# Optimization experiments

Hardware: AMD Instinct MI355X
Metric: run time of the kernel (lower is better)

The kernel has to match this reference:

```python
import jax, jax.numpy as jnp
import numpy as np
from jax.ops import segment_sum

N_V = 50000   # vertices
N_E = 10000   # hyperedges
N_P = 800000  # incidence pairs
D_IN = 256
D_OUT = 256
NEG_SLOPE = 0.01


def setup_inputs() -> dict:
    key = jax.random.key(0)
    k1, k2, k3, k4, k5 = jax.random.split(key, 5)
    X = jax.random.normal(k1, (N_V, D_IN), dtype=jnp.float32)
    W = jax.random.normal(k2, (D_IN, D_OUT), dtype=jnp.float32) * (1.0 / np.sqrt(D_IN))
    b = jax.random.normal(k3, (D_OUT,), dtype=jnp.float32) * 0.01
    v_idx = jax.random.randint(k4, (N_P,), 0, N_V, dtype=jnp.int32)
    e_idx = jax.random.randint(k5, (N_P,), 0, N_E, dtype=jnp.int32)
    return {"X": X, "W": W, "b": b, "v_idx": v_idx, "e_idx": e_idx,
            "num_hyperedges": N_E}


def _mean_scatter(msg, idx, num_segments):
    # segment mean with count clamped to >=1 (empty segments -> 0)
    s = segment_sum(msg, idx, num_segments=num_segments)
    cnt = segment_sum(jnp.ones((msg.shape[0],), msg.dtype), idx,
                      num_segments=num_segments)
    return s / jnp.maximum(cnt, 1.0)[:, None]


def reference(X, W, b, v_idx, e_idx, num_hyperedges):
    # theta: linear projection  [N_V, D_OUT]
    H = X @ W + b
    # v2e mean: hyperedge features from member vertices
    e_feat = _mean_scatter(H[v_idx], e_idx, num_hyperedges)   # [N_E, D_OUT]
    # e2v mean: vertex features from incident hyperedges
    v_feat = _mean_scatter(e_feat[e_idx], v_idx, X.shape[0])  # [N_V, D_OUT]
    # leaky relu, default negative slope 0.01
    return jnp.where(v_feat >= 0, v_feat, NEG_SLOPE * v_feat)
```

## Files before the change

### kernel.cpp

```cpp
#include <hip/hip_runtime.h>

#define D 256
#define NEG_SLOPE 0.01f
#define E_PAD 192
#define V_PAD 64
#define EB 32
#define VB 64
#define NBE 313
#define NBV 782
#define CAP_E 3328
#define CAP_V 1536
#define CHUNK 1024
#define CR (CHUNK/256)
#define NS 8
#define DS 32
#define NSE 2
#define DSE 128

__device__ __forceinline__ unsigned short f2bf(float f) {
    union { float f; unsigned u; } x; x.f = f;
    unsigned r = x.u + 0x7fffu + ((x.u >> 16) & 1u);
    return (unsigned short)(r >> 16);
}
__device__ __forceinline__ void acc8(float* acc, uint4 g) {
    union { unsigned u; float f; } t;
    t.u = g.x << 16;         acc[0] += t.f;
    t.u = g.x & 0xffff0000u; acc[1] += t.f;
    t.u = g.y << 16;         acc[2] += t.f;
    t.u = g.y & 0xffff0000u; acc[3] += t.f;
    t.u = g.z << 16;         acc[4] += t.f;
    t.u = g.z & 0xffff0000u; acc[5] += t.f;
    t.u = g.w << 16;         acc[6] += t.f;
    t.u = g.w & 0xffff0000u; acc[7] += t.f;
}

__global__ __launch_bounds__(256) void prep_kernel(
        const float* __restrict__ X, unsigned short* __restrict__ Xhs,
        const int* __restrict__ v_idx, const int* __restrict__ e_idx,
        int* __restrict__ bc_e, int* __restrict__ bc_v,
        unsigned* __restrict__ pe, unsigned* __restrict__ pv,
        int n_v, int n_p, int gp) {
    __shared__ int he[NBE], hv[NBV], beb[NBE], bvb[NBV];
    const int tid = threadIdx.x;
    if ((int)blockIdx.x < gp) {
        const int base = (int)blockIdx.x * CHUNK;
        int le[CR], lv[CR];
        for (int i = tid; i < NBE; i += 256) he[i] = 0;
        for (int i = tid; i < NBV; i += 256) hv[i] = 0;
        __syncthreads();
        #pragma unroll
        for (int r = 0; r < CR; ++r) {
            int p = base + r * 256 + tid;
            le[r] = -1; lv[r] = -1;
            if (p < n_p) {
                le[r] = e_idx[p]; lv[r] = v_idx[p];
                atomicAdd(&he[le[r] >> 5], 1);
                atomicAdd(&hv[lv[r] >> 6], 1);
            }
        }
        __syncthreads();
        for (int b = tid; b < NBE; b += 256) {
            int c = he[b];
            beb[b] = c ? atomicAdd(&bc_e[b], c) : 0;
            he[b] = 0;
        }
        for (int b = tid; b < NBV; b += 256) {
            int c = hv[b];
            bvb[b] = c ? atomicAdd(&bc_v[b], c) : 0;
            hv[b] = 0;
        }
        __syncthreads();
        #pragma unroll
        for (int r = 0; r < CR; ++r) {
            if (le[r] >= 0) {
                int e = le[r], v = lv[r];
                int b1 = e >> 5;
                int s1 = beb[b1] + atomicAdd(&he[b1], 1);
                if (s1 < CAP_E) pe[(size_t)b1 * CAP_E + s1] = (unsigned)v | ((unsigned)e << 16);
                int b2 = v >> 6;
                int s2 = bvb[b2] + atomicAdd(&hv[b2], 1);
                if (s2 < CAP_V) pv[(size_t)b2 * CAP_V + s2] = (unsigned)e | ((unsigned)v << 16);
            }
        }
    } else {
        int i = ((int)blockIdx.x - gp) * 256 + tid;
        if (i >= n_v * 64) return;
        int v = i >> 6;
        int d4 = (i & 63) * 4;
        float4 val = *(const float4*)(X + (size_t)v * D + d4);
        ushort4 h;
        h.x = f2bf(val.x); h.y = f2bf(val.y); h.z = f2bf(val.z); h.w = f2bf(val.w);
        int s = d4 >> 5, wd = d4 & 31;
        *(ushort4*)(Xhs + (size_t)s * n_v * DS + (size_t)v * DS + wd) = h;
    }
}

__global__ __launch_bounds__(256) void build_kernel(
        const unsigned* __restrict__ pe, const unsigned* __restrict__ pv,
        const int* __restrict__ bc_e, const int* __restrict__ bc_v,
        unsigned short* __restrict__ e_adj, int* __restrict__ e_fill,
        unsigned short* __restrict__ v_adj, int* __restrict__ v_fill,
        int n_e, int n_v) {
    __shared__ unsigned short adj[EB * E_PAD];
    __shared__ int cnt[VB];
    const int tid = threadIdx.x;
    if ((int)blockIdx.x < NBE) {
        const int b = blockIdx.x;
        const int e0 = b * EB;
        int m = n_e - e0; if (m > EB) m = EB;
        for (int i = tid; i < EB; i += 256) cnt[i] = 0;
        __syncthreads();
        int total = bc_e[b]; if (total > CAP_E) total = CAP_E;
        for (int i = tid; i < total; i += 256) {
            unsigned p = pe[(size_t)b * CAP_E + i];
            int v = (int)(p & 0xFFFFu);
            int el = (int)(p >> 16) - e0;
            int s = atomicAdd(&cnt[el], 1);
            if (s < E_PAD) adj[el * E_PAD + s] = (unsigned short)v;
        }
        __syncthreads();
        unsigned* gout = (unsigned*)(e_adj + (size_t)e0 * E_PAD);
        const unsigned* lin = (const unsigned*)adj;
        int words = m * E_PAD / 2;
        for (int j = tid; j < words; j += 256) gout[j] = lin[j];
        for (int el = tid; el < m; el += 256) {
            int c = cnt[el]; if (c > E_PAD) c = E_PAD;
            e_fill[e0 + el] = c;
        }
    } else {
        const int b = (int)blockIdx.x - NBE;
        const int v0 = b * VB;
        int m = n_v - v0; if (m > VB) m = VB;
        for (int i = tid; i < VB; i += 256) cnt[i] = 0;
        __syncthreads();
        int total = bc_v[b]; if (total > CAP_V) total = CAP_V;
        for (int i = tid; i < total; i += 256) {
            unsigned p = pv[(size_t)b * CAP_V + i];
            int e = (int)(p & 0xFFFFu);
            int vl = (int)(p >> 16) - v0;
            int s = atomicAdd(&cnt[vl], 1);
            if (s < V_PAD) adj[vl * V_PAD + s] = (unsigned short)e;
        }
        __syncthreads();
        unsigned* gout = (unsigned*)(v_adj + (size_t)v0 * V_PAD);
        const unsigned* lin = (const unsigned*)adj;
        int words = m * V_PAD / 2;
        for (int j = tid; j < words; j += 256) gout[j] = lin[j];
        for (int vl = tid; vl < m; vl += 256) {
            int c = cnt[vl]; if (c > V_PAD) c = V_PAD;
            v_fill[v0 + vl] = c;
        }
    }
}

__global__ __launch_bounds__(256) void v2e_kernel(
        const unsigned short* __restrict__ Xhs, const int* __restrict__ e_fill,
        const unsigned short* __restrict__ e_adj, float* __restrict__ Xagg,
        int n_e, int n_v) {
    const int s    = blockIdx.x;
    const int eg   = threadIdx.x >> 4;
    const int l16  = threadIdx.x & 15;
    const int ph   = l16 >> 2;
    const int sub  = l16 & 3;
    const int e    = blockIdx.y * 16 + eg;
    if (e >= n_e) return;
    const unsigned short* tab = Xhs + (size_t)s * n_v * DS + (sub << 3);
    const unsigned short* adj = e_adj + (size_t)e * E_PAD;
    int cnt = e_fill[e]; if (cnt > E_PAD) cnt = E_PAD;
    float acc[8] = {};
    int i = ph * 4;
    for (; i + 4 <= cnt; i += 16) {
        ushort4 A = *(const ushort4*)(adj + i);
        uint4 g0 = *(const uint4*)(tab + (size_t)A.x * DS);
        uint4 g1 = *(const uint4*)(tab + (size_t)A.y * DS);
        uint4 g2 = *(const uint4*)(tab + (size_t)A.z * DS);
        uint4 g3 = *(const uint4*)(tab + (size_t)A.w * DS);
        acc8(acc, g0); acc8(acc, g1); acc8(acc, g2); acc8(acc, g3);
    }
    for (int j = i; j < cnt; ++j) {
        uint4 g = *(const uint4*)(tab + (size_t)adj[j] * DS);
        acc8(acc, g);
    }
    #pragma unroll
    for (int k = 0; k < 8; ++k) {
        acc[k] += __shfl_xor(acc[k], 4);
        acc[k] += __shfl_xor(acc[k], 8);
    }
    if (ph == 0) {
        int c = cnt < 1 ? 1 : cnt;
        float inv = 1.0f / (float)c;
        float4 o0, o1;
        o0.x = acc[0] * inv; o0.y = acc[1] * inv; o0.z = acc[2] * inv; o0.w = acc[3] * inv;
        o1.x = acc[4] * inv; o1.y = acc[5] * inv; o1.z = acc[6] * inv; o1.w = acc[7] * inv;
        float* orow = Xagg + (size_t)e * D + s * DS + (sub << 3);
        *(float4*)(orow)     = o0;
        *(float4*)(orow + 4) = o1;
    }
}

#define BM 64
#define BN 64
#define BK 64
#define SAK 68
#define SBN 68

__global__ __launch_bounds__(256) void gemm_kernel(
        const float* __restrict__ A, const float* __restrict__ B,
        const float* __restrict__ bias, const int* __restrict__ e_cnt,
        unsigned short* __restrict__ Ehs, int M) {
    __shared__ float As[BM * SAK];
    __shared__ float Bs[BK * SBN];
    const int tid = threadIdx.x;
    const int tx = tid & 15, ty = tid >> 4;
    const int m0 = blockIdx.y * BM;
    const int n0 = blockIdx.x * BN;

    float acc[4][4] = {};

    for (int k0 = 0; k0 < D; k0 += BK) {
        #pragma unroll
        for (int r = 0; r < 4; ++r) {
            int l  = (tid + r * 256) * 4;
            int am = l >> 6;
            int ak = l & 63;
            int grow = m0 + am;
            float4 v = make_float4(0.f, 0.f, 0.f, 0.f);
            if (grow < M) v = *(const float4*)(A + (size_t)grow * D + k0 + ak);
            *(float4*)(&As[am * SAK + ak]) = v;
        }
        #pragma unroll
        for (int r = 0; r < 4; ++r) {
            int l  = (tid + r * 256) * 4;
            int bk = l >> 6;
            int bn = l & 63;
            float4 v = *(const float4*)(B + (size_t)(k0 + bk) * D + n0 + bn);
            *(float4*)(&Bs[bk * SBN + bn]) = v;
        }
        __syncthreads();

        #pragma unroll 8
        for (int kk = 0; kk < BK; ++kk) {
            float a0 = As[(ty * 4 + 0) * SAK + kk];
            float a1 = As[(ty * 4 + 1) * SAK + kk];
            float a2 = As[(ty * 4 + 2) * SAK + kk];
            float a3 = As[(ty * 4 + 3) * SAK + kk];
            float4 bv = *(const float4*)(Bs + kk * SBN + tx * 4);
            acc[0][0] += a0 * bv.x; acc[0][1] += a0 * bv.y; acc[0][2] += a0 * bv.z; acc[0][3] += a0 * bv.w;
            acc[1][0] += a1 * bv.x; acc[1][1] += a1 * bv.y; acc[1][2] += a1 * bv.z; acc[1][3] += a1 * bv.w;
            acc[2][0] += a2 * bv.x; acc[2][1] += a2 * bv.y; acc[2][2] += a2 * bv.z; acc[2][3] += a2 * bv.w;
            acc[3][0] += a3 * bv.x; acc[3][1] += a3 * bv.y; acc[3][2] += a3 * bv.z; acc[3][3] += a3 * bv.w;
        }
        __syncthreads();
    }

    float4 bb = *(const float4*)(bias + n0 + tx * 4);
    const int dcol = n0 + tx * 4;
    const int ss = dcol >> 7, wd = dcol & 127;
    #pragma unroll
    for (int i = 0; i < 4; ++i) {
        int row = m0 + ty * 4 + i;
        if (row < M) {
            bool nonempty = e_cnt[row] > 0;
            ushort4 o;
            o.x = f2bf(nonempty ? acc[i][0] + bb.x : 0.f);
            o.y = f2bf(nonempty ? acc[i][1] + bb.y : 0.f);
            o.z = f2bf(nonempty ? acc[i][2] + bb.z : 0.f);
            o.w = f2bf(nonempty ? acc[i][3] + bb.w : 0.f);
            *(ushort4*)(Ehs + (size_t)ss * M * DSE + (size_t)row * DSE + wd) = o;
        }
    }
}

__global__ __launch_bounds__(256) void e2v_kernel(
        const unsigned short* __restrict__ Ehs, const unsigned short* __restrict__ v_adj,
        const int* __restrict__ v_fill, float* __restrict__ out, int n_v, int n_e) {
    const int s   = blockIdx.x;
    const int grp = threadIdx.x >> 4;
    const int sub = threadIdx.x & 15;
    const int v   = blockIdx.y * 16 + grp;
    if (v >= n_v) return;
    const unsigned short* tab = Ehs + (size_t)s * n_e * DSE + (sub << 3);
    const unsigned short* a   = v_adj + (size_t)v * V_PAD;
    int c = v_fill[v]; if (c > V_PAD) c = V_PAD;
    float acc[8] = {};
    int i = 0;
    for (; i + 8 <= c; i += 8) {
        ushort4 E0 = *(const ushort4*)(a + i);
        ushort4 E1 = *(const ushort4*)(a + i + 4);
        uint4 g0 = *(const uint4*)(tab + (size_t)E0.x * DSE);
        uint4 g1 = *(const uint4*)(tab + (size_t)E0.y * DSE);
        uint4 g2 = *(const uint4*)(tab + (size_t)E0.z * DSE);
        uint4 g3 = *(const uint4*)(tab + (size_t)E0.w * DSE);
        uint4 g4 = *(const uint4*)(tab + (size_t)E1.x * DSE);
        uint4 g5 = *(const uint4*)(tab + (size_t)E1.y * DSE);
        uint4 g6 = *(const uint4*)(tab + (size_t)E1.z * DSE);
        uint4 g7 = *(const uint4*)(tab + (size_t)E1.w * DSE);
        acc8(acc, g0); acc8(acc, g1); acc8(acc, g2); acc8(acc, g3);
        acc8(acc, g4); acc8(acc, g5); acc8(acc, g6); acc8(acc, g7);
    }
    for (; i < c; ++i) {
        uint4 g = *(const uint4*)(tab + (size_t)a[i] * DSE);
        acc8(acc, g);
    }
    int cc = c < 1 ? 1 : c;
    float inv = 1.0f / (float)cc;
    float4 o0, o1;
    #pragma unroll
    for (int k = 0; k < 8; ++k) acc[k] *= inv;
    o0.x = acc[0] >= 0.f ? acc[0] : NEG_SLOPE * acc[0];
    o0.y = acc[1] >= 0.f ? acc[1] : NEG_SLOPE * acc[1];
    o0.z = acc[2] >= 0.f ? acc[2] : NEG_SLOPE * acc[2];
    o0.w = acc[3] >= 0.f ? acc[3] : NEG_SLOPE * acc[3];
    o1.x = acc[4] >= 0.f ? acc[4] : NEG_SLOPE * acc[4];
    o1.y = acc[5] >= 0.f ? acc[5] : NEG_SLOPE * acc[5];
    o1.z = acc[6] >= 0.f ? acc[6] : NEG_SLOPE * acc[6];
    o1.w = acc[7] >= 0.f ? acc[7] : NEG_SLOPE * acc[7];
    float* orow = out + (size_t)v * D + s * DSE + (sub << 3);
    *(float4*)(orow)     = o0;
    *(float4*)(orow + 4) = o1;
}

extern "C" void kernel_launch(void* const* d_in, const int* in_sizes, int n_in,
                              void* d_out, int out_size, void* d_ws, size_t ws_size,
                              hipStream_t stream) {
    const float* X    = (const float*)d_in[0];
    const float* W    = (const float*)d_in[1];
    const float* bias = (const float*)d_in[2];
    const int* v_idx  = (const int*)d_in[3];
    const int* e_idx  = (const int*)d_in[4];
    const int n_v = in_sizes[0] / D;
    const int n_p = in_sizes[3];
    const int n_e = 10000;

    char* w = (char*)d_ws;
    size_t off = 0;
    auto alloc = [&](size_t bytes) -> void* {
        void* p = w + off;
        off = (off + bytes + 255) & ~(size_t)255;
        return p;
    };
    unsigned short* Xhs = (unsigned short*)alloc((size_t)NS * n_v * DS * sizeof(unsigned short));
    float* Xagg         = (float*)alloc((size_t)n_e * D * sizeof(float));
    unsigned short* Ehs = (unsigned short*)alloc((size_t)n_e * D * sizeof(unsigned short));
    unsigned short* e_adj = (unsigned short*)alloc((size_t)n_e * E_PAD * sizeof(unsigned short));
    unsigned short* v_adj = (unsigned short*)alloc((size_t)n_v * V_PAD * sizeof(unsigned short));
    unsigned* pe   = (unsigned*)alloc((size_t)NBE * CAP_E * sizeof(unsigned));
    unsigned* pv   = (unsigned*)alloc((size_t)NBV * CAP_V * sizeof(unsigned));
    int* fills     = (int*)alloc((size_t)(n_e + n_v) * sizeof(int));
    int* e_fill = fills;
    int* v_fill = fills + n_e;
    int* bc        = (int*)alloc((size_t)(NBE + NBV) * sizeof(int));
    int* bc_e = bc;
    int* bc_v = bc + NBE;

    hipMemsetAsync(bc, 0, (size_t)(NBE + NBV) * sizeof(int), stream);

    int gp = (n_p + CHUNK - 1) / CHUNK;
    int gc = (n_v * 64 + 255) / 256;
    prep_kernel<<<gp + gc, 256, 0, stream>>>(X, Xhs, v_idx, e_idx,
                                             bc_e, bc_v, pe, pv, n_v, n_p, gp);

    build_kernel<<<NBE + NBV, 256, 0, stream>>>(pe, pv, bc_e, bc_v,
                                                e_adj, e_fill, v_adj, v_fill,
                                                n_e, n_v);

    dim3 vgrid(NS, (n_e + 15) / 16);
    v2e_kernel<<<vgrid, 256, 0, stream>>>(Xhs, e_fill, e_adj, Xagg, n_e, n_v);

    dim3 ggrid(D / BN, (n_e + BM - 1) / BM);
    gemm_kernel<<<ggrid, 256, 0, stream>>>(Xagg, W, bias, e_fill, Ehs, n_e);

    dim3 egrid(NSE, (n_v + 15) / 16);
    e2v_kernel<<<egrid, 256, 0, stream>>>(Ehs, v_adj, v_fill, (float*)d_out, n_v, n_e);
}
```

Before: 258.8 us.

## Replace global atomic bucket offsets with per-block fixed-capacity bucket segments

The prep kernel now writes each incidence pair straight into a fixed-size per-(chunk, bucket) slot region instead of taking global atomic offsets. This removes the second pass, the global atomics and the memset, and the chunk size is doubled. The build kernel then walks every chunk's segment for its bucket, using per-chunk counts. Staging buffers are aliased into the aggregation workspace and the output buffer to save memory. In exchange, build reads many mostly empty slots, and pairs are silently dropped if a chunk overflows a bucket's small capacity (32 or 16 slots).

```diff
diff --git a/kernel.cpp b/kernel.cpp
--- a/kernel.cpp
+++ b/kernel.cpp
@@ -8,10 +8,11 @@
 #define VB 64
 #define NBE 313
 #define NBV 782
-#define CAP_E 3328
-#define CAP_V 1536
-#define CHUNK 1024
+#define CHUNK 2048
 #define CR (CHUNK/256)
+#define CAPE 32
+#define CAPV 16
+#define MAXNPB 1024
 #define NS 8
 #define DS 32
 #define NSE 2
@@ -37,50 +38,40 @@
 __global__ __launch_bounds__(256) void prep_kernel(
         const float* __restrict__ X, unsigned short* __restrict__ Xhs,
         const int* __restrict__ v_idx, const int* __restrict__ e_idx,
-        int* __restrict__ bc_e, int* __restrict__ bc_v,
+        int* __restrict__ cnt_e, int* __restrict__ cnt_v,
         unsigned* __restrict__ pe, unsigned* __restrict__ pv,
         int n_v, int n_p, int gp) {
-    __shared__ int he[NBE], hv[NBV], beb[NBE], bvb[NBV];
+    __shared__ int he[NBE], hv[NBV];
     const int tid = threadIdx.x;
     if ((int)blockIdx.x < gp) {
-        const int base = (int)blockIdx.x * CHUNK;
-        int le[CR], lv[CR];
+        const int blk  = blockIdx.x;
+        const int base = blk * CHUNK;
         for (int i = tid; i < NBE; i += 256) he[i] = 0;
         for (int i = tid; i < NBV; i += 256) hv[i] = 0;
         __syncthreads();
         #pragma unroll
         for (int r = 0; r < CR; ++r) {
             int p = base + r * 256 + tid;
-            le[r] = -1; lv[r] = -1;
             if (p < n_p) {
-                le[r] = e_idx[p]; lv[r] = v_idx[p];
-                atomicAdd(&he[le[r] >> 5], 1);
-                atomicAdd(&hv[lv[r] >> 6], 1);
+                int e = e_idx[p], v = v_idx[p];
+                int b1 = e >> 5;
+                int s1 = atomicAdd(&he[b1], 1);
+                if (s1 < CAPE)
+                    pe[(((size_t)blk * NBE + b1) << 5) + s1] = (unsigned)v | ((unsigned)e << 16);
+                int b2 = v >> 6;
+                int s2 = atomicAdd(&hv[b2], 1);
+                if (s2 < CAPV)
+                    pv[(((size_t)blk * NBV + b2) << 4) + s2] = (unsigned)e | ((unsigned)v << 16);
             }
         }
         __syncthreads();
         for (int b = tid; b < NBE; b += 256) {
-            int c = he[b];
-            beb[b] = c ? atomicAdd(&bc_e[b], c) : 0;
-            he[b] = 0;
+            int c = he[b]; if (c > CAPE) c = CAPE;
+            cnt_e[(size_t)blk * NBE + b] = c;
         }
         for (int b = tid; b < NBV; b += 256) {
-            int c = hv[b];
-            bvb[b] = c ? atomicAdd(&bc_v[b], c) : 0;
-            hv[b] = 0;
-        }
-        __syncthreads();
-        #pragma unroll
-        for (int r = 0; r < CR; ++r) {
-            if (le[r] >= 0) {
-                int e = le[r], v = lv[r];
-                int b1 = e >> 5;
-                int s1 = beb[b1] + atomicAdd(&he[b1], 1);
-                if (s1 < CAP_E) pe[(size_t)b1 * CAP_E + s1] = (unsigned)v | ((unsigned)e << 16);
-                int b2 = v >> 6;
-                int s2 = bvb[b2] + atomicAdd(&hv[b2], 1);
-                if (s2 < CAP_V) pv[(size_t)b2 * CAP_V + s2] = (unsigned)e | ((unsigned)v << 16);
-            }
+            int c = hv[b]; if (c > CAPV) c = CAPV;
+            cnt_v[(size_t)blk * NBV + b] = c;
         }
     } else {
         int i = ((int)blockIdx.x - gp) * 256 + tid;
@@ -97,26 +88,31 @@
 
 __global__ __launch_bounds__(256) void build_kernel(
         const unsigned* __restrict__ pe, const unsigned* __restrict__ pv,
-        const int* __restrict__ bc_e, const int* __restrict__ bc_v,
+        const int* __restrict__ cnt_e, const int* __restrict__ cnt_v,
         unsigned short* __restrict__ e_adj, int* __restrict__ e_fill,
         unsigned short* __restrict__ v_adj, int* __restrict__ v_fill,
-        int n_e, int n_v) {
+        int n_e, int n_v, int npb) {
     __shared__ unsigned short adj[EB * E_PAD];
     __shared__ int cnt[VB];
+    __shared__ int scnt[MAXNPB];
     const int tid = threadIdx.x;
     if ((int)blockIdx.x < NBE) {
         const int b = blockIdx.x;
         const int e0 = b * EB;
         int m = n_e - e0; if (m > EB) m = EB;
         for (int i = tid; i < EB; i += 256) cnt[i] = 0;
-        __syncthreads();
-        int total = bc_e[b]; if (total > CAP_E) total = CAP_E;
-        for (int i = tid; i < total; i += 256) {
-            unsigned p = pe[(size_t)b * CAP_E + i];
-            int v = (int)(p & 0xFFFFu);
-            int el = (int)(p >> 16) - e0;
-            int s = atomicAdd(&cnt[el], 1);
-            if (s < E_PAD) adj[el * E_PAD + s] = (unsigned short)v;
+        for (int j = tid; j < npb; j += 256) scnt[j] = cnt_e[(size_t)j * NBE + b];
+        __syncthreads();
+        int total = npb << 5;
+        for (int f = tid; f < total; f += 256) {
+            int seg = f >> 5, slot = f & 31;
+            if (slot < scnt[seg]) {
+                unsigned p = pe[(((size_t)seg * NBE + b) << 5) + slot];
+                int v = (int)(p & 0xFFFFu);
+                int el = (int)(p >> 16) - e0;
+                int s = atomicAdd(&cnt[el], 1);
+                if (s < E_PAD) adj[el * E_PAD + s] = (unsigned short)v;
+            }
         }
         __syncthreads();
         unsigned* gout = (unsigned*)(e_adj + (size_t)e0 * E_PAD);
@@ -132,14 +128,18 @@
         const int v0 = b * VB;
         int m = n_v - v0; if (m > VB) m = VB;
         for (int i = tid; i < VB; i += 256) cnt[i] = 0;
-        __syncthreads();
-        int total = bc_v[b]; if (total > CAP_V) total = CAP_V;
-        for (int i = tid; i < total; i += 256) {
-            unsigned p = pv[(size_t)b * CAP_V + i];
-            int e = (int)(p & 0xFFFFu);
-            int vl = (int)(p >> 16) - v0;
-            int s = atomicAdd(&cnt[vl], 1);
-            if (s < V_PAD) adj[vl * V_PAD + s] = (unsigned short)e;
+        for (int j = tid; j < npb; j += 256) scnt[j] = cnt_v[(size_t)j * NBV + b];
+        __syncthreads();
+        int total = npb << 4;
+        for (int f = tid; f < total; f += 256) {
+            int seg = f >> 4, slot = f & 15;
+            if (slot < scnt[seg]) {
+                unsigned p = pv[(((size_t)seg * NBV + b) << 4) + slot];
+                int e = (int)(p & 0xFFFFu);
+                int vl = (int)(p >> 16) - v0;
+                int s = atomicAdd(&cnt[vl], 1);
+                if (s < V_PAD) adj[vl * V_PAD + s] = (unsigned short)e;
+            }
         }
         __syncthreads();
         unsigned* gout = (unsigned*)(v_adj + (size_t)v0 * V_PAD);
@@ -332,6 +332,9 @@
     const int n_p = in_sizes[3];
     const int n_e = 10000;
 
+    int gp = (n_p + CHUNK - 1) / CHUNK;
+    if (gp > MAXNPB) gp = MAXNPB;
+
     char* w = (char*)d_ws;
     size_t off = 0;
     auto alloc = [&](size_t bytes) -> void* {
@@ -340,29 +343,30 @@
         return p;
     };
     unsigned short* Xhs = (unsigned short*)alloc((size_t)NS * n_v * DS * sizeof(unsigned short));
-    float* Xagg         = (float*)alloc((size_t)n_e * D * sizeof(float));
-    unsigned short* Ehs = (unsigned short*)alloc((size_t)n_e * D * sizeof(unsigned short));
+    size_t pe_bytes  = (size_t)gp * NBE * CAPE * sizeof(unsigned);
+    size_t agg_bytes = (size_t)n_e * D * sizeof(float);
+    size_t ehs_bytes = (size_t)n_e * D * sizeof(unsigned short);
+    size_t uni_bytes = pe_bytes > agg_bytes + ehs_bytes ? pe_bytes : agg_bytes + ehs_bytes;
+    char* uni = (char*)alloc(uni_bytes);
+    unsigned* pe        = (unsigned*)uni;
+    float* Xagg         = (float*)uni;
+    unsigned short* Ehs = (unsigned short*)(uni + agg_bytes);
+    unsigned* pv        = (unsigned*)d_out;
     unsigned short* e_adj = (unsigned short*)alloc((size_t)n_e * E_PAD * sizeof(unsigned short));
     unsigned short* v_adj = (unsigned short*)alloc((size_t)n_v * V_PAD * sizeof(unsigned short));
-    unsigned* pe   = (unsigned*)alloc((size_t)NBE * CAP_E * sizeof(unsigned));
-    unsigned* pv   = (unsigned*)alloc((size_t)NBV * CAP_V * sizeof(unsigned));
+    int* cnt_e     = (int*)alloc((size_t)gp * NBE * sizeof(int));
+    int* cnt_v     = (int*)alloc((size_t)gp * NBV * sizeof(int));
     int* fills     = (int*)alloc((size_t)(n_e + n_v) * sizeof(int));
     int* e_fill = fills;
     int* v_fill = fills + n_e;
-    int* bc        = (int*)alloc((size_t)(NBE + NBV) * sizeof(int));
-    int* bc_e = bc;
-    int* bc_v = bc + NBE;
-
-    hipMemsetAsync(bc, 0, (size_t)(NBE + NBV) * sizeof(int), stream);
-
-    int gp = (n_p + CHUNK - 1) / CHUNK;
+
     int gc = (n_v * 64 + 255) / 256;
     prep_kernel<<<gp + gc, 256, 0, stream>>>(X, Xhs, v_idx, e_idx,
-                                             bc_e, bc_v, pe, pv, n_v, n_p, gp);
-
-    build_kernel<<<NBE + NBV, 256, 0, stream>>>(pe, pv, bc_e, bc_v,
+                                             cnt_e, cnt_v, pe, pv, n_v, n_p, gp);
+
+    build_kernel<<<NBE + NBV, 256, 0, stream>>>(pe, pv, cnt_e, cnt_v,
                                                 e_adj, e_fill, v_adj, v_fill,
-                                                n_e, n_v);
+                                                n_e, n_v, gp);
 
     dim3 vgrid(NS, (n_e + 15) / 16);
     v2e_kernel<<<vgrid, 256, 0, stream>>>(Xhs, e_fill, e_adj, Xagg, n_e, n_v);
```

Measured after the change: 260.9 us. Within noise of the previous version (+0.8%).
